# Kernel tuning notes

Measured on AMD Instinct MI355X. Metric: run time of the kernel, lower is better.

## Reference

```python
import jax, jax.numpy as jnp
import numpy as np


def setup_inputs() -> dict:
    key = jax.random.key(0)
    k1, k2, k3, k4, k5 = jax.random.split(key, 5)
    B, C, T, U = 4, 256, 4096, 64
    y1 = jax.random.normal(k1, (B, C, T), dtype=jnp.float32)
    y2 = jax.random.normal(k2, (B, C, T), dtype=jnp.float32)
    # module init: uniform(-0.02, 0.02)
    Wq = jax.random.uniform(k3, (C, U), minval=-0.02, maxval=0.02, dtype=jnp.float32)
    Wk = jax.random.uniform(k4, (C, U), minval=-0.02, maxval=0.02, dtype=jnp.float32)
    Wv = jax.random.uniform(k5, (C, U), minval=-0.02, maxval=0.02, dtype=jnp.float32)
    return {"y1": y1, "y2": y2, "Wq": Wq, "Wk": Wk, "Wv": Wv, "attention_width": 256}


def reference(y1, y2, Wq, Wk, Wv, attention_width):
    # y1, y2: [B, C, T] -> projected to [B, T, U]
    q1 = jnp.einsum('bct,cu->btu', y1, Wq)
    k2 = jnp.einsum('bct,cu->btu', y2, Wk)
    v2 = jnp.einsum('bct,cu->btu', y2, Wv)
    d_k = q1.shape[-1]
    # scores e[b, i, j] = q1[b,i,:] . k2[b,j,:] / sqrt(U)
    e = jnp.einsum('biu,bju->bij', q1, k2) / jnp.sqrt(jnp.float32(d_k))
    T = e.shape[-1]
    # banded mask: keep (i, j) where j - w//2 <= i < j - w//2 + w
    lower = jnp.arange(T) - attention_width // 2          # [T] (per column j)
    upper = lower + attention_width                        # [T]
    i = jnp.arange(T)[:, None]                             # [T, 1] (row index)
    mask = (lower <= i) & (i < upper)                      # [T, T]
    e = jnp.where(mask, e, -jnp.inf)
    a = jax.nn.softmax(e, axis=-1)                         # [B, T, T]
    # out = (a @ v2) then permute(0, 2, 1) -> [B, U, T]
    out = jnp.einsum('bij,bju->bui', a, v2)
    return (out, a)
```

## Files before the change

kernel.cpp:

```cpp
#include <hip/hip_runtime.h>

using uint = unsigned int;
typedef unsigned short ushort_t;
typedef float f32x4 __attribute__((ext_vector_type(4)));
typedef short short8 __attribute__((ext_vector_type(8)));

#define B_ 4
#define C_ 256
#define T_ 4096
#define U_ 64

static __device__ __forceinline__ float bflo(uint w) { return __uint_as_float(w << 16); }
static __device__ __forceinline__ float bfhi(uint w) { return __uint_as_float(w & 0xffff0000u); }
static __device__ __forceinline__ uint f2bf(float f) {
    uint x = __float_as_uint(f);
    return (x + 0x7fffu + ((x >> 16) & 1u)) >> 16;
}

__global__ __launch_bounds__(256) void wconv_kernel(
    const float* __restrict__ Wq, const float* __restrict__ Wk,
    const float* __restrict__ Wv, ushort_t* __restrict__ WT)
{
    const int m = blockIdx.x >> 3;
    const int q = blockIdx.x & 7;
    const float* W = (m == 0) ? Wq : (m == 1) ? Wk : Wv;
    int g  = q * 256 + threadIdx.x;
    int u  = g >> 5;
    int c8 = (g & 31) << 3;
    short8 o;
#pragma unroll
    for (int j = 0; j < 8; ++j)
        o[j] = (short)f2bf(W[(size_t)(c8 + j) * U_ + u]);
    *(short8*)(WT + ((size_t)m * U_ + u) * C_ + c8) = o;
}

__global__ __launch_bounds__(256) void proj_kernel(
    const float* __restrict__ y1, const float* __restrict__ y2,
    const ushort_t* __restrict__ WT,
    ushort_t* __restrict__ Qb, ushort_t* __restrict__ Kb, ushort_t* __restrict__ Vt)
{
    __shared__ alignas(16) ushort_t wt[2][64][264];

    const int bid = blockIdx.x;
    const int tid = threadIdx.x;
    const int p   = bid & 1;
    const int bq2 = bid >> 1;
    const int b   = bq2 >> 6;
    const int t0  = (bq2 & 63) << 6;
    const int wid = tid >> 6, l = tid & 63;
    const int lm  = l & 15, lg = l >> 4;

    {
        const ushort_t* s0 = WT + (size_t)(p == 0 ? 0 : 1) * (U_ * C_);
        const ushort_t* s1 = WT + (size_t)2 * (U_ * C_);
#pragma unroll
        for (int it = 0; it < 8; ++it) {
            int idx = it * 256 + tid;
            int u = idx >> 5, c8 = (idx & 31) << 3;
            *(short8*)&wt[0][u][c8] = *(const short8*)(s0 + u * C_ + c8);
            if (p)
                *(short8*)&wt[1][u][c8] = *(const short8*)(s1 + u * C_ + c8);
        }
    }
    __syncthreads();

    const float* ysrc = ((p == 0) ? y1 : y2) + (size_t)b * (C_ * T_);
    const float* yp   = ysrc + (size_t)(8 * lg) * T_ + (t0 + 16 * wid + lm);

    f32x4 acc0[4] = {};
    f32x4 acc1[4] = {};
#pragma unroll
    for (int ks = 0; ks < 8; ++ks) {
        float av[8];
#pragma unroll
        for (int j = 0; j < 8; ++j)
            av[j] = yp[(size_t)(32 * ks + j) * T_];
        short8 af;
#pragma unroll
        for (int j = 0; j < 8; ++j)
            af[j] = (short)f2bf(av[j]);
#pragma unroll
        for (int n = 0; n < 4; ++n) {
            short8 bq = *(const short8*)&wt[0][16 * n + lm][32 * ks + 8 * lg];
            acc0[n] = __builtin_amdgcn_mfma_f32_16x16x32_bf16(af, bq, acc0[n], 0, 0, 0);
            if (p) {
                short8 bv = *(const short8*)&wt[1][16 * n + lm][32 * ks + 8 * lg];
                acc1[n] = __builtin_amdgcn_mfma_f32_16x16x32_bf16(af, bv, acc1[n], 0, 0, 0);
            }
        }
    }

    ushort_t* O0 = p ? Kb : Qb;
#pragma unroll
    for (int n = 0; n < 4; ++n)
#pragma unroll
        for (int r = 0; r < 4; ++r) {
            int t = t0 + 16 * wid + 4 * lg + r;
            int u = 16 * n + lm;
            O0[((size_t)b * T_ + t) * U_ + u] = (ushort_t)f2bf(acc0[n][r]);
            if (p)
                Vt[((size_t)b * U_ + u) * T_ + t] = (ushort_t)f2bf(acc1[n][r]);
        }
}

__global__ __launch_bounds__(256, 3) void attn_kernel(
    const ushort_t* __restrict__ Qb, const ushort_t* __restrict__ Kb,
    const ushort_t* __restrict__ Vt, float* __restrict__ gout)
{
    __shared__ alignas(16) ushort_t vt[64][296];
    __shared__ alignas(16) ushort_t alds[16][296];
    __shared__ float sums[4][4][4];

    const int bid = blockIdx.x;
    const int b   = bid >> 8;
    const int i0  = (bid & 255) << 4;
    const int tid = threadIdx.x;
    const int w   = tid >> 6, l = tid & 63;
    const int lm  = l & 15, lg = l >> 4;

    const int jb2    = max(0, i0 - 127) & ~7;
    const int jend   = min(T_, i0 + 144);
    const int width2 = jend - jb2;
    const int NT     = (width2 + 15) >> 4;

    {
        const int su = tid >> 2;
        const int c0 = tid & 3;
        const ushort_t* vrow = Vt + ((size_t)b * U_ + su) * T_ + jb2;
#pragma unroll
        for (int k = 0; k < 9; ++k) {
            int c = c0 + 4 * k;
            short8 v = {};
            if (8 * c < width2)
                v = *(const short8*)(vrow + 8 * c);
            *(short8*)&vt[su][8 * c] = v;
        }
    }

    const ushort_t* qrow = Qb + ((size_t)b * T_ + i0 + lm) * U_ + 8 * lg;
    const short8 aq0 = *(const short8*)(qrow);
    const short8 aq1 = *(const short8*)(qrow + 32);

    const int ivec = i0 + 4 * lg;
    f32x4 ev[5];
    f32x4 psum = {};
#pragma unroll
    for (int s = 0; s < 5; ++s) {
        const int jt = 4 * s + w;
        ev[s] = (f32x4)(0.f);
        if (jt < 18) {
            const int j    = jb2 + 16 * jt + lm;
            const int krow = min(j, T_ - 1);
            const ushort_t* kp = Kb + ((size_t)b * T_ + krow) * U_ + 8 * lg;
            short8 bk0 = *(const short8*)(kp);
            short8 bk1 = *(const short8*)(kp + 32);
            f32x4 acc = {};
            acc = __builtin_amdgcn_mfma_f32_16x16x32_bf16(aq0, bk0, acc, 0, 0, 0);
            acc = __builtin_amdgcn_mfma_f32_16x16x32_bf16(aq1, bk1, acc, 0, 0, 0);
#pragma unroll
            for (int r = 0; r < 4; ++r) {
                int i = ivec + r;
                bool valid = (j >= i - 127) && (j <= i + 128) && (j < T_);
                float e = valid ? __expf(acc[r] * 0.125f) : 0.f;
                ev[s][r] = e;
                psum[r] += e;
            }
        }
    }
#pragma unroll
    for (int m = 1; m < 16; m <<= 1) {
#pragma unroll
        for (int r = 0; r < 4; ++r)
            psum[r] += __shfl_xor(psum[r], m, 64);
    }
    if (lm == 0)
        *(f32x4*)&sums[w][lg][0] = psum;
    __syncthreads();

    f32x4 rtot = *(f32x4*)&sums[0][lg][0];
    rtot += *(f32x4*)&sums[1][lg][0];
    rtot += *(f32x4*)&sums[2][lg][0];
    rtot += *(f32x4*)&sums[3][lg][0];
    f32x4 rinv;
#pragma unroll
    for (int r = 0; r < 4; ++r)
        rinv[r] = __builtin_amdgcn_rcpf(rtot[r]);

    f32x4 av[5];
#pragma unroll
    for (int s = 0; s < 5; ++s) {
        const int jt = 4 * s + w;
        if (jt < 18) {
#pragma unroll
            for (int r = 0; r < 4; ++r) {
                float a = ev[s][r] * rinv[r];
                av[s][r] = a;
                alds[4 * lg + r][16 * jt + lm] = (ushort_t)f2bf(a);
            }
        }
    }
    __syncthreads();

    float* aout = gout + (size_t)B_ * U_ * T_;
#pragma unroll
    for (int s = 0; s < 5; ++s) {
        const int jt = 4 * s + w;
        if (jt < 18) {
            const int j = jb2 + 16 * jt + lm;
#pragma unroll
            for (int r = 0; r < 4; ++r) {
                int i = ivec + r;
                if ((j >= i - 127) && (j <= i + 128) && (j < T_))
                    __builtin_nontemporal_store(av[s][r],
                        aout + ((size_t)b * T_ + i) * T_ + j);
            }
        }
    }
    {
        const f32x4 zz = (f32x4)(0.f);
#pragma unroll
        for (int rr = 0; rr < 4; ++rr) {
            const int i   = i0 + 4 * w + rr;
            const int jlo = max(0, i - 127);
            const int jhi = min(T_ - 1, i + 128);
            float* rowp = aout + ((size_t)b * T_ + i) * T_;
            f32x4* row4 = (f32x4*)rowp;
            int nleft4 = jlo >> 2;
            for (int k = l; k < nleft4; k += 64)
                __builtin_nontemporal_store(zz, row4 + k);
            int rem = jlo & 3;
            if (l < rem)
                __builtin_nontemporal_store(0.f, rowp + (jlo & ~3) + l);
            int js = jhi + 1;
            int ah = (4 - (js & 3)) & 3;
            if (l < ah && js + l < T_)
                __builtin_nontemporal_store(0.f, rowp + js + l);
            int js4 = (js + ah) >> 2;
            for (int k = js4 + l; k < T_ / 4; k += 64)
                __builtin_nontemporal_store(zz, row4 + k);
        }
    }

    f32x4 pacc = {};
#pragma unroll
    for (int kc = 0; kc < 9; ++kc) {
        short8 pa = *(const short8*)&alds[lm][8 * lg + 32 * kc];
        short8 pb = *(const short8*)&vt[16 * w + lm][8 * lg + 32 * kc];
        pacc = __builtin_amdgcn_mfma_f32_16x16x32_bf16(pa, pb, pacc, 0, 0, 0);
    }
#pragma unroll
    for (int r = 0; r < 4; ++r)
        gout[((size_t)b * U_ + 16 * w + lm) * T_ + i0 + 4 * lg + r] = pacc[r];
}

extern "C" void kernel_launch(void* const* d_in, const int* in_sizes, int n_in,
                              void* d_out, int out_size, void* d_ws, size_t ws_size,
                              hipStream_t stream)
{
    const float* y1 = (const float*)d_in[0];
    const float* y2 = (const float*)d_in[1];
    const float* Wq = (const float*)d_in[2];
    const float* Wk = (const float*)d_in[3];
    const float* Wv = (const float*)d_in[4];

    ushort_t* Qb = (ushort_t*)d_ws;
    ushort_t* Kb = Qb + (size_t)B_ * T_ * U_;
    ushort_t* Vt = Kb + (size_t)B_ * T_ * U_;
    ushort_t* WT = Vt + (size_t)B_ * T_ * U_;

    float* gout = (float*)d_out;

    wconv_kernel<<<24, 256, 0, stream>>>(Wq, Wk, Wv, WT);
    proj_kernel<<<512, 256, 0, stream>>>(y1, y2, WT, Qb, Kb, Vt);
    attn_kernel<<<1024, 256, 0, stream>>>(Qb, Kb, Vt, gout);
}
```

Baseline: 91.76 us.

## Fold weight conversion into projection and widen attention blocks to 32 query rows

```diff
diff --git a/kernel.cpp b/kernel.cpp
--- a/kernel.cpp
+++ b/kernel.cpp
@@ -17,52 +17,40 @@
     return (x + 0x7fffu + ((x >> 16) & 1u)) >> 16;
 }
 
-__global__ __launch_bounds__(256) void wconv_kernel(
-    const float* __restrict__ Wq, const float* __restrict__ Wk,
-    const float* __restrict__ Wv, ushort_t* __restrict__ WT)
-{
-    const int m = blockIdx.x >> 3;
-    const int q = blockIdx.x & 7;
-    const float* W = (m == 0) ? Wq : (m == 1) ? Wk : Wv;
-    int g  = q * 256 + threadIdx.x;
-    int u  = g >> 5;
-    int c8 = (g & 31) << 3;
-    short8 o;
-#pragma unroll
-    for (int j = 0; j < 8; ++j)
-        o[j] = (short)f2bf(W[(size_t)(c8 + j) * U_ + u]);
-    *(short8*)(WT + ((size_t)m * U_ + u) * C_ + c8) = o;
-}
-
 __global__ __launch_bounds__(256) void proj_kernel(
     const float* __restrict__ y1, const float* __restrict__ y2,
-    const ushort_t* __restrict__ WT,
+    const float* __restrict__ Wq, const float* __restrict__ Wk,
+    const float* __restrict__ Wv,
     ushort_t* __restrict__ Qb, ushort_t* __restrict__ Kb, ushort_t* __restrict__ Vt)
 {
     __shared__ alignas(16) ushort_t wt[2][64][264];
 
-    const int bid = blockIdx.x;
+    const int p   = blockIdx.y;
+    const int b   = blockIdx.x >> 6;
+    const int t0  = (blockIdx.x & 63) << 6;
     const int tid = threadIdx.x;
-    const int p   = bid & 1;
-    const int bq2 = bid >> 1;
-    const int b   = bq2 >> 6;
-    const int t0  = (bq2 & 63) << 6;
+
+    {
+        const float* W0 = (p == 0) ? Wq : Wk;
+#pragma unroll
+        for (int k = 0; k < 64; ++k) {
+            int idx = tid + 256 * k;
+            int c = idx >> 6, u = idx & 63;
+            wt[0][u][c] = (ushort_t)f2bf(W0[idx]);
+        }
+        if (p == 1) {
+#pragma unroll
+            for (int k = 0; k < 64; ++k) {
+                int idx = tid + 256 * k;
+                int c = idx >> 6, u = idx & 63;
+                wt[1][u][c] = (ushort_t)f2bf(Wv[idx]);
+            }
+        }
+    }
+    __syncthreads();
+
     const int wid = tid >> 6, l = tid & 63;
-    const int lm  = l & 15, lg = l >> 4;
-
-    {
-        const ushort_t* s0 = WT + (size_t)(p == 0 ? 0 : 1) * (U_ * C_);
-        const ushort_t* s1 = WT + (size_t)2 * (U_ * C_);
-#pragma unroll
-        for (int it = 0; it < 8; ++it) {
-            int idx = it * 256 + tid;
-            int u = idx >> 5, c8 = (idx & 31) << 3;
-            *(short8*)&wt[0][u][c8] = *(const short8*)(s0 + u * C_ + c8);
-            if (p)
-                *(short8*)&wt[1][u][c8] = *(const short8*)(s1 + u * C_ + c8);
-        }
-    }
-    __syncthreads();
+    const int lm = l & 15, lg = l >> 4;
 
     const float* ysrc = ((p == 0) ? y1 : y2) + (size_t)b * (C_ * T_);
     const float* yp   = ysrc + (size_t)(8 * lg) * T_ + (t0 + 16 * wid + lm);
@@ -103,65 +91,89 @@
         }
 }
 
-__global__ __launch_bounds__(256, 3) void attn_kernel(
+__global__ __launch_bounds__(512) void attn_kernel(
     const ushort_t* __restrict__ Qb, const ushort_t* __restrict__ Kb,
     const ushort_t* __restrict__ Vt, float* __restrict__ gout)
 {
+    __shared__ alignas(16) uint     kw[288 * 32];
     __shared__ alignas(16) ushort_t vt[64][296];
-    __shared__ alignas(16) ushort_t alds[16][296];
-    __shared__ float sums[4][4][4];
+    __shared__ alignas(16) ushort_t alds[32][296];
+    __shared__ alignas(16) uint     qlds[32][32];
+    __shared__ float sums[8][20];
 
     const int bid = blockIdx.x;
-    const int b   = bid >> 8;
-    const int i0  = (bid & 255) << 4;
+    const int b   = bid >> 7;
+    const int i0  = (bid & 127) << 5;
     const int tid = threadIdx.x;
-    const int w   = tid >> 6, l = tid & 63;
-    const int lm  = l & 15, lg = l >> 4;
 
     const int jb2    = max(0, i0 - 127) & ~7;
-    const int jend   = min(T_, i0 + 144);
+    const int jend   = min(T_, i0 + 160);
     const int width2 = jend - jb2;
-    const int NT     = (width2 + 15) >> 4;
-
-    {
-        const int su = tid >> 2;
-        const int c0 = tid & 3;
-        const ushort_t* vrow = Vt + ((size_t)b * U_ + su) * T_ + jb2;
-#pragma unroll
-        for (int k = 0; k < 9; ++k) {
-            int c = c0 + 4 * k;
-            short8 v = {};
-            if (8 * c < width2)
-                v = *(const short8*)(vrow + 8 * c);
-            *(short8*)&vt[su][8 * c] = v;
-        }
-    }
-
-    const ushort_t* qrow = Qb + ((size_t)b * T_ + i0 + lm) * U_ + 8 * lg;
-    const short8 aq0 = *(const short8*)(qrow);
-    const short8 aq1 = *(const short8*)(qrow + 32);
-
-    const int ivec = i0 + 4 * lg;
+    const int NT     = width2 >> 4;
+
+    for (int idx = tid; idx < 2304; idx += 512) {
+        int row = idx >> 3, q = idx & 7;
+        int srow = min(jb2 + row, T_ - 1);
+        uint4 v = ((const uint4*)(Kb + ((size_t)b * T_ + srow) * U_))[q];
+        *(uint4*)(kw + row * 32 + ((4 * q) ^ ((row & 7) << 2))) = v;
+    }
+    {
+        const int u = tid >> 3, c0 = tid & 7;
+        const ushort_t* vrow = Vt + ((size_t)b * U_ + u) * T_ + jb2;
+#pragma unroll
+        for (int k = 0; k < 5; ++k) {
+            int c = c0 + 8 * k;
+            if (c < 37) {
+                short8 v = {};
+                if (8 * c < width2)
+                    v = *(const short8*)(vrow + 8 * c);
+                *(short8*)&vt[u][8 * c] = v;
+            }
+        }
+    }
+    if (tid < 256) {
+        const int row = tid >> 3, q = tid & 7;
+        uint4 v = ((const uint4*)(Qb + ((size_t)b * T_ + i0 + row) * U_))[q];
+        *(uint4*)&qlds[row][(4 * q) ^ ((row & 7) << 2)] = v;
+    }
+    {
+        short8 z = {};
+        short8* af = (short8*)&alds[0][0];
+        for (int idx = tid; idx < 1184; idx += 512)
+            af[idx] = z;
+    }
+    __syncthreads();
+
+    const int w = tid >> 6, l = tid & 63;
+    const int lm = l & 15, lg = l >> 4;
+    const int qt = w & 1, jt0 = w >> 1;
+    const int selq = (lm & 7) << 2;
+
+    const uint* qr = &qlds[16 * qt + lm][0];
+    const short8 aq0 = *(const short8*)(qr + ((4 * lg) ^ selq));
+    const short8 aq1 = *(const short8*)(qr + ((16 + 4 * lg) ^ selq));
+
     f32x4 ev[5];
     f32x4 psum = {};
 #pragma unroll
+    for (int s = 0; s < 5; ++s) ev[s] = (f32x4)(0.f);
+#pragma unroll
     for (int s = 0; s < 5; ++s) {
-        const int jt = 4 * s + w;
-        ev[s] = (f32x4)(0.f);
-        if (jt < 18) {
-            const int j    = jb2 + 16 * jt + lm;
-            const int krow = min(j, T_ - 1);
-            const ushort_t* kp = Kb + ((size_t)b * T_ + krow) * U_ + 8 * lg;
-            short8 bk0 = *(const short8*)(kp);
-            short8 bk1 = *(const short8*)(kp + 32);
+        const int jt = 4 * s + jt0;
+        if (jt < NT) {
+            const int row = 16 * jt + lm;
+            const uint* kr = kw + row * 32;
+            short8 bk0 = *(const short8*)(kr + ((4 * lg) ^ selq));
+            short8 bk1 = *(const short8*)(kr + ((16 + 4 * lg) ^ selq));
             f32x4 acc = {};
             acc = __builtin_amdgcn_mfma_f32_16x16x32_bf16(aq0, bk0, acc, 0, 0, 0);
             acc = __builtin_amdgcn_mfma_f32_16x16x32_bf16(aq1, bk1, acc, 0, 0, 0);
+            const int j = jb2 + row;
 #pragma unroll
             for (int r = 0; r < 4; ++r) {
-                int i = ivec + r;
-                bool valid = (j >= i - 127) && (j <= i + 128) && (j < T_);
-                float e = valid ? __expf(acc[r] * 0.125f) : 0.f;
+                int i = i0 + 16 * qt + 4 * lg + r;
+                bool val = (j >= i - 127) && (j <= i + 128);
+                float e = val ? __expf(acc[r] * 0.125f) : 0.f;
                 ev[s][r] = e;
                 psum[r] += e;
             }
@@ -174,44 +186,44 @@
             psum[r] += __shfl_xor(psum[r], m, 64);
     }
     if (lm == 0)
-        *(f32x4*)&sums[w][lg][0] = psum;
-    __syncthreads();
-
-    f32x4 rtot = *(f32x4*)&sums[0][lg][0];
-    rtot += *(f32x4*)&sums[1][lg][0];
-    rtot += *(f32x4*)&sums[2][lg][0];
-    rtot += *(f32x4*)&sums[3][lg][0];
+        *(f32x4*)&sums[w][4 * lg] = psum;
+    __syncthreads();
+
+    f32x4 rtot = *(const f32x4*)&sums[qt][4 * lg];
+    rtot += *(const f32x4*)&sums[qt + 2][4 * lg];
+    rtot += *(const f32x4*)&sums[qt + 4][4 * lg];
+    rtot += *(const f32x4*)&sums[qt + 6][4 * lg];
     f32x4 rinv;
 #pragma unroll
     for (int r = 0; r < 4; ++r)
         rinv[r] = __builtin_amdgcn_rcpf(rtot[r]);
 
-    f32x4 av[5];
 #pragma unroll
     for (int s = 0; s < 5; ++s) {
-        const int jt = 4 * s + w;
-        if (jt < 18) {
+        const int jt = 4 * s + jt0;
+        if (jt < NT) {
 #pragma unroll
             for (int r = 0; r < 4; ++r) {
                 float a = ev[s][r] * rinv[r];
-                av[s][r] = a;
-                alds[4 * lg + r][16 * jt + lm] = (ushort_t)f2bf(a);
+                ev[s][r] = a;
+                alds[16 * qt + 4 * lg + r][16 * jt + lm] = (ushort_t)f2bf(a);
             }
         }
     }
     __syncthreads();
 
     float* aout = gout + (size_t)B_ * U_ * T_;
+
 #pragma unroll
     for (int s = 0; s < 5; ++s) {
-        const int jt = 4 * s + w;
-        if (jt < 18) {
+        const int jt = 4 * s + jt0;
+        if (jt < NT) {
             const int j = jb2 + 16 * jt + lm;
 #pragma unroll
             for (int r = 0; r < 4; ++r) {
-                int i = ivec + r;
-                if ((j >= i - 127) && (j <= i + 128) && (j < T_))
-                    __builtin_nontemporal_store(av[s][r],
+                int i = i0 + 16 * qt + 4 * lg + r;
+                if ((j >= i - 127) && (j <= i + 128))
+                    __builtin_nontemporal_store(ev[s][r],
                         aout + ((size_t)b * T_ + i) * T_ + j);
             }
         }
@@ -241,16 +253,19 @@
         }
     }
 
-    f32x4 pacc = {};
-#pragma unroll
-    for (int kc = 0; kc < 9; ++kc) {
-        short8 pa = *(const short8*)&alds[lm][8 * lg + 32 * kc];
-        short8 pb = *(const short8*)&vt[16 * w + lm][8 * lg + 32 * kc];
-        pacc = __builtin_amdgcn_mfma_f32_16x16x32_bf16(pa, pb, pacc, 0, 0, 0);
-    }
-#pragma unroll
-    for (int r = 0; r < 4; ++r)
-        gout[((size_t)b * U_ + 16 * w + lm) * T_ + i0 + 4 * lg + r] = pacc[r];
+    {
+        const int wu = w >> 1, qp = w & 1;
+        f32x4 pacc = {};
+#pragma unroll
+        for (int kc = 0; kc < 9; ++kc) {
+            short8 pa = *(const short8*)&vt[16 * wu + lm][8 * lg + 32 * kc];
+            short8 pb = *(const short8*)&alds[16 * qp + lm][8 * lg + 32 * kc];
+            pacc = __builtin_amdgcn_mfma_f32_16x16x32_bf16(pa, pb, pacc, 0, 0, 0);
+        }
+#pragma unroll
+        for (int r = 0; r < 4; ++r)
+            gout[((size_t)b * U_ + 16 * wu + 4 * lg + r) * T_ + i0 + 16 * qp + lm] = pacc[r];
+    }
 }
 
 extern "C" void kernel_launch(void* const* d_in, const int* in_sizes, int n_in,
@@ -266,11 +281,9 @@
     ushort_t* Qb = (ushort_t*)d_ws;
     ushort_t* Kb = Qb + (size_t)B_ * T_ * U_;
     ushort_t* Vt = Kb + (size_t)B_ * T_ * U_;
-    ushort_t* WT = Vt + (size_t)B_ * T_ * U_;
 
     float* gout = (float*)d_out;
 
-    wconv_kernel<<<24, 256, 0, stream>>>(Wq, Wk, Wv, WT);
-    proj_kernel<<<512, 256, 0, stream>>>(y1, y2, WT, Qb, Kb, Vt);
-    attn_kernel<<<1024, 256, 0, stream>>>(Qb, Kb, Vt, gout);
-}
+    proj_kernel<<<dim3(B_ * (T_ / 64), 2), 256, 0, stream>>>(y1, y2, Wq, Wk, Wv, Qb, Kb, Vt);
+    attn_kernel<<<512, 512, 0, stream>>>(Qb, Kb, Vt, gout);
+}
```

New measurement: 86.10 us. 1.07x faster.
